# Kernel tuning notes

Hardware: AMD Instinct MI355X
Metric: run time of the kernel (lower is better)

The kernel has to match this reference:

```python
import jax, jax.numpy as jnp
import numpy as np

GAMMA, ZETA = -0.1, 1.1
N_BITS = 4
QMAX = (1 << N_BITS) - 1  # 15
OUT, IN, D, K = 4096, 4096, 8, 4096
L = (OUT * IN) // D  # 2097152 blocks, no padding needed


def setup_inputs() -> dict:
    key = jax.random.key(0)
    k = jax.random.split(key, 7)
    x = jax.random.normal(k[0], (4, 2048, IN), jnp.float32)
    codebook = jax.random.normal(k[1], (K, D), jnp.float32)
    indices = jax.random.randint(k[2], (L,), 0, K, jnp.int32)
    base_int = jax.random.randint(k[3], (OUT, IN), 0, QMAX, jnp.int32)
    scale = jax.random.uniform(k[4], (OUT, 1), jnp.float32)
    zero = jax.random.uniform(k[5], (OUT, 1), jnp.float32)
    bias = jax.random.normal(k[6], (OUT,), jnp.float32)
    return {"x": x, "codebook": codebook, "indices": indices,
            "base_int": base_int, "scale": scale, "zero": zero, "bias": bias}


def reference(x, codebook, indices, base_int, scale, zero, bias):
    # Gather codebook blocks and rebuild alpha with the weight's shape [OUT, IN]
    alpha = codebook[indices].reshape(OUT, IN)
    # Rectified sigmoid (soft quant mode)
    r = jnp.clip(jax.nn.sigmoid(alpha) * (ZETA - GAMMA) + GAMMA, 0.0, 1.0)
    # Affine int-quant reconstruction
    q_int = jnp.clip(base_int.astype(scale.dtype) + r + zero, 0.0, float(QMAX))
    Wq = scale * (q_int - zero)  # [OUT, IN]
    # F.linear: x @ Wq^T + bias
    return jnp.einsum('bsi,oi->bso', x, Wq) + bias
```

## Files before the change

kernel.cpp:

```cpp
#include <hip/hip_runtime.h>

#define M_DIM 8192
#define N_DIM 4096
#define K_DIM 4096
#define L_BLK 2097152
#define K2 8192

typedef __attribute__((ext_vector_type(8))) short short8;
typedef __attribute__((ext_vector_type(8))) unsigned short ushort8;
typedef __attribute__((ext_vector_type(4))) float f32x4;

__device__ __forceinline__ unsigned short f2bf(float f) {
  unsigned int u = __float_as_uint(f);
  unsigned int r = (u + 0x7fffu + ((u >> 16) & 1u)) >> 16;
  return (unsigned short)r;
}

__device__ __forceinline__ void gld16(const void* g, void* l) {
  __builtin_amdgcn_global_load_lds(
      (const __attribute__((address_space(1))) void*)g,
      (__attribute__((address_space(3))) void*)l, 16, 0, 0);
}

__global__ void dequant_kernel(const float* __restrict__ cb,
                               const int* __restrict__ idx,
                               const int* __restrict__ base,
                               const float* __restrict__ scale,
                               const float* __restrict__ zero,
                               unsigned short* __restrict__ W) {
  const int b = blockIdx.x * 256 + threadIdx.x;
  const int o = b >> 9;
  const float s = scale[o];
  const float z = zero[o];
  const int ci = idx[b];
  const float4* crow = (const float4*)(cb + (size_t)ci * 8);
  float4 c0 = crow[0], c1 = crow[1];
  const int4* brow = (const int4*)(base + (size_t)b * 8);
  int4 b0 = brow[0], b1 = brow[1];
  float a[8]  = {c0.x, c0.y, c0.z, c0.w, c1.x, c1.y, c1.z, c1.w};
  int   bi[8] = {b0.x, b0.y, b0.z, b0.w, b1.x, b1.y, b1.z, b1.w};
  union { unsigned short h[8]; ushort8 v; } u;
#pragma unroll
  for (int d = 0; d < 8; ++d) {
    float sg = 1.0f / (1.0f + __expf(-a[d]));
    float r = fminf(fmaxf(sg * 1.2f - 0.1f, 0.0f), 1.0f);
    float q = fminf(fmaxf((float)bi[d] + r + z, 0.0f), 15.0f);
    u.h[d] = f2bf(s * (q - z));
  }
  *(ushort8*)(W + (size_t)b * 8) = u.v;
}

__global__ void xconv_kernel(const float* __restrict__ x,
                             unsigned short* __restrict__ xb) {
  const size_t i = (size_t)blockIdx.x * 256 + threadIdx.x;
  const float4* X = (const float4*)x;
  float4 a0 = X[i * 2], a1 = X[i * 2 + 1];
  float f[8] = {a0.x, a0.y, a0.z, a0.w, a1.x, a1.y, a1.z, a1.w};
  union { unsigned short h[8]; ushort8 v; } u;
#pragma unroll
  for (int d = 0; d < 8; ++d) u.h[d] = f2bf(f[d]);
  *(ushort8*)(xb + i * 8) = u.v;
}


#define VMW(N) asm volatile("s_waitcnt vmcnt(" #N ")" ::: "memory")
#define BAR __builtin_amdgcn_s_barrier()

#define RDB(BF, BUFO) \
  _Pragma("unroll") for (int n = 0; n < 4; ++n) \
  _Pragma("unroll") for (int kk = 0; kk < 2; ++kk) \
    BF[n][kk] = *(const short8*)(lds + (BUFO) + 32768 + \
        (wn * 64 + n * 16 + r16) * 128 + (acol0 ^ (kk << 6)));

#define RDA(AF, BUFO, P) \
  _Pragma("unroll") for (int mi = 0; mi < 2; ++mi) \
  _Pragma("unroll") for (int kk = 0; kk < 2; ++kk) \
    AF[mi][kk] = *(const short8*)(lds + (BUFO) + \
        (wm * 128 + (2 * (P) + mi) * 16 + r16) * 128 + (acol0 ^ (kk << 6)));

#define FMQ(P, AF, BF) do { \
  __builtin_amdgcn_s_setprio(1); \
  _Pragma("unroll") for (int kk = 0; kk < 2; ++kk) \
  _Pragma("unroll") for (int mi = 0; mi < 2; ++mi) \
  _Pragma("unroll") for (int n = 0; n < 4; ++n) \
    acc[2 * (P) + mi][n] = __builtin_amdgcn_mfma_f32_16x16x32_bf16( \
        AF[mi][kk], BF[n][kk], acc[2 * (P) + mi][n], 0, 0, 0); \
  __builtin_amdgcn_s_setprio(0); \
} while (0)

#define ITER(CUR, NXT, T) do { \
   RDA(afA, CUR, 0); RDB(bf, CUR); \
  stA(NXT, 1, (T) + 1); stA(NXT, 3, (T) + 1); \
  BAR; FMQ(0, afA, bf); BAR; \
   RDA(afB, CUR, 1); \
  stB(CUR, 0, (T) + 2); stB(CUR, 1, (T) + 2); \
  BAR; FMQ(1, afB, bf); BAR; \
   RDA(afA, CUR, 2); \
  stB(CUR, 2, (T) + 2); stB(CUR, 3, (T) + 2); \
  BAR; FMQ(2, afA, bf); BAR; \
   RDA(afB, CUR, 3); \
  stA(CUR, 0, (T) + 2); stA(CUR, 2, (T) + 2); \
  VMW(6); BAR; FMQ(3, afB, bf); BAR; \
} while (0)

__global__ __launch_bounds__(512, 2)
void gemm_bt(const unsigned short* __restrict__ A,
             const unsigned short* __restrict__ B,
             const float* __restrict__ bias,
             float* __restrict__ C) {
  __shared__ char lds[131072];
  const int tid = threadIdx.x;
  const int lane = tid & 63;
  const int w = tid >> 6;
  const int wm = w >> 2;
  const int wn = w & 3;
  const int r16 = lane & 15;
  const int g = lane >> 4;
  const int acol0 = (g << 4) ^ ((r16 & 7) << 4);

  const int s = (int)blockIdx.x;
  const int wg = (s & 7) * 64 + (s >> 3);
  const int bm = wg & 31;
  const int bn = wg >> 5;

  const char* Abase = (const char*)A + (size_t)bm * 256 * K2;
  const char* Bbase = (const char*)B + (size_t)bn * 256 * K2;

  const int strow = tid >> 3;
  const int scol = ((tid & 7) * 16) ^ ((strow & 7) << 4);
  const int sdst = w * 1024;

  auto stA = [&](int bo, int c, int kt) {
    gld16(Abase + (size_t)(c * 64 + strow) * K2 + kt * 128 + scol,
          lds + bo + c * 8192 + sdst);
  };
  auto stB = [&](int bo, int c, int kt) {
    gld16(Bbase + (size_t)(c * 64 + strow) * K2 + kt * 128 + scol,
          lds + bo + 32768 + c * 8192 + sdst);
  };

  f32x4 acc[8][4] = {};
  short8 bf[4][2];
  short8 afA[2][2], afB[2][2];

  stB(0, 0, 0); stB(0, 1, 0); stB(0, 2, 0); stB(0, 3, 0);
  stA(0, 0, 0); stA(0, 1, 0); stA(0, 2, 0); stA(0, 3, 0);
  stB(65536, 0, 1); stB(65536, 1, 1); stB(65536, 2, 1); stB(65536, 3, 1);
  stA(65536, 0, 1); stA(65536, 2, 1);
  VMW(6); BAR;

  for (int tp = 0; tp < 31; ++tp) {
    ITER(0, 65536, 2 * tp);
    ITER(65536, 0, 2 * tp + 1);
  }
  RDA(afA, 0, 0); RDB(bf, 0);
  stA(65536, 1, 63); stA(65536, 3, 63);
  BAR; FMQ(0, afA, bf); BAR;
  RDA(afB, 0, 1);
  BAR; FMQ(1, afB, bf); BAR;
  RDA(afA, 0, 2);
  BAR; FMQ(2, afA, bf); BAR;
  RDA(afB, 0, 3);
  VMW(0); BAR; FMQ(3, afB, bf); BAR;
  RDA(afA, 65536, 0); RDB(bf, 65536);
  FMQ(0, afA, bf);
  RDA(afB, 65536, 1);
  FMQ(1, afB, bf);
  RDA(afA, 65536, 2);
  FMQ(2, afA, bf);
  RDA(afB, 65536, 3);
  FMQ(3, afB, bf);

  const int cb0 = bn * 256 + wn * 64 + r16;
  float bv[4];
#pragma unroll
  for (int n = 0; n < 4; ++n) bv[n] = bias[cb0 + n * 16];
#pragma unroll
  for (int m = 0; m < 8; ++m) {
#pragma unroll
    for (int j = 0; j < 4; ++j) {
      int row = bm * 256 + wm * 128 + m * 16 + g * 4 + j;
      float* Crow = C + (size_t)row * N_DIM + cb0;
#pragma unroll
      for (int n = 0; n < 4; ++n) Crow[n * 16] = acc[m][n][j] + bv[n];
    }
  }
}

extern "C" void kernel_launch(void* const* d_in, const int* in_sizes, int n_in,
                              void* d_out, int out_size, void* d_ws, size_t ws_size,
                              hipStream_t stream) {
  const float* x     = (const float*)d_in[0];
  const float* cb    = (const float*)d_in[1];
  const int*   idx   = (const int*)d_in[2];
  const int*   base  = (const int*)d_in[3];
  const float* scale = (const float*)d_in[4];
  const float* zero  = (const float*)d_in[5];
  const float* bias  = (const float*)d_in[6];
  float* out = (float*)d_out;

  unsigned short* Wq = (unsigned short*)d_ws;
  unsigned short* Xb = (unsigned short*)((char*)d_ws + (size_t)N_DIM * K_DIM * 2);

  dequant_kernel<<<L_BLK / 256, 256, 0, stream>>>(cb, idx, base, scale, zero, Wq);
  xconv_kernel<<<(M_DIM * K_DIM / 8) / 256, 256, 0, stream>>>(x, Xb);
  gemm_bt<<<(M_DIM / 256) * (N_DIM / 256), 512, 0, stream>>>(Xb, Wq, bias, out);
}
```

Baseline: 310.6 us.

## Merge prep kernels and switch GEMM to 4 waves with 128x128 warp tiles

Fuses the weight dequant and x bf16 conversion into one launch, which removes a kernel boundary. The GEMM drops from 8 waves to 4 per 256x256 tile. Each wave now computes a 128x128 sub-tile with 8x8 accumulators, and each thread issues two async global-to-LDS loads per stage. This raises per-wave register reuse of A/B fragments and cuts LDS read traffic per MFMA, at the cost of heavy VGPR pressure (256 accumulator floats) and fewer waves for hiding latency.

```diff
diff --git a/kernel.cpp b/kernel.cpp
--- a/kernel.cpp
+++ b/kernel.cpp
@@ -22,88 +22,89 @@
       (__attribute__((address_space(3))) void*)l, 16, 0, 0);
 }
 
-__global__ void dequant_kernel(const float* __restrict__ cb,
-                               const int* __restrict__ idx,
-                               const int* __restrict__ base,
-                               const float* __restrict__ scale,
-                               const float* __restrict__ zero,
-                               unsigned short* __restrict__ W) {
-  const int b = blockIdx.x * 256 + threadIdx.x;
-  const int o = b >> 9;
-  const float s = scale[o];
-  const float z = zero[o];
-  const int ci = idx[b];
-  const float4* crow = (const float4*)(cb + (size_t)ci * 8);
-  float4 c0 = crow[0], c1 = crow[1];
-  const int4* brow = (const int4*)(base + (size_t)b * 8);
-  int4 b0 = brow[0], b1 = brow[1];
-  float a[8]  = {c0.x, c0.y, c0.z, c0.w, c1.x, c1.y, c1.z, c1.w};
-  int   bi[8] = {b0.x, b0.y, b0.z, b0.w, b1.x, b1.y, b1.z, b1.w};
-  union { unsigned short h[8]; ushort8 v; } u;
-#pragma unroll
-  for (int d = 0; d < 8; ++d) {
-    float sg = 1.0f / (1.0f + __expf(-a[d]));
-    float r = fminf(fmaxf(sg * 1.2f - 0.1f, 0.0f), 1.0f);
-    float q = fminf(fmaxf((float)bi[d] + r + z, 0.0f), 15.0f);
-    u.h[d] = f2bf(s * (q - z));
+__global__ void prep_kernel(const float* __restrict__ cb,
+                            const int* __restrict__ idx,
+                            const int* __restrict__ base,
+                            const float* __restrict__ scale,
+                            const float* __restrict__ zero,
+                            const float* __restrict__ x,
+                            unsigned short* __restrict__ W,
+                            unsigned short* __restrict__ xb) {
+  if (blockIdx.x < L_BLK / 256) {
+    const int b = blockIdx.x * 256 + threadIdx.x;
+    const int o = b >> 9;
+    const float s = scale[o];
+    const float z = zero[o];
+    const int ci = idx[b];
+    const float4* crow = (const float4*)(cb + (size_t)ci * 8);
+    float4 c0 = crow[0], c1 = crow[1];
+    const int4* brow = (const int4*)(base + (size_t)b * 8);
+    int4 b0 = brow[0], b1 = brow[1];
+    float a[8]  = {c0.x, c0.y, c0.z, c0.w, c1.x, c1.y, c1.z, c1.w};
+    int   bi[8] = {b0.x, b0.y, b0.z, b0.w, b1.x, b1.y, b1.z, b1.w};
+    union { unsigned short h[8]; ushort8 v; } u;
+#pragma unroll
+    for (int d = 0; d < 8; ++d) {
+      float sg = 1.0f / (1.0f + __expf(-a[d]));
+      float r = fminf(fmaxf(sg * 1.2f - 0.1f, 0.0f), 1.0f);
+      float q = fminf(fmaxf((float)bi[d] + r + z, 0.0f), 15.0f);
+      u.h[d] = f2bf(s * (q - z));
+    }
+    *(ushort8*)(W + (size_t)b * 8) = u.v;
+  } else {
+    const size_t i = (size_t)(blockIdx.x - L_BLK / 256) * 256 + threadIdx.x;
+    const float4* X = (const float4*)x;
+    float4 a0 = X[i * 2], a1 = X[i * 2 + 1];
+    float f[8] = {a0.x, a0.y, a0.z, a0.w, a1.x, a1.y, a1.z, a1.w};
+    union { unsigned short h[8]; ushort8 v; } u;
+#pragma unroll
+    for (int d = 0; d < 8; ++d) u.h[d] = f2bf(f[d]);
+    *(ushort8*)(xb + i * 8) = u.v;
   }
-  *(ushort8*)(W + (size_t)b * 8) = u.v;
-}
-
-__global__ void xconv_kernel(const float* __restrict__ x,
-                             unsigned short* __restrict__ xb) {
-  const size_t i = (size_t)blockIdx.x * 256 + threadIdx.x;
-  const float4* X = (const float4*)x;
-  float4 a0 = X[i * 2], a1 = X[i * 2 + 1];
-  float f[8] = {a0.x, a0.y, a0.z, a0.w, a1.x, a1.y, a1.z, a1.w};
-  union { unsigned short h[8]; ushort8 v; } u;
-#pragma unroll
-  for (int d = 0; d < 8; ++d) u.h[d] = f2bf(f[d]);
-  *(ushort8*)(xb + i * 8) = u.v;
 }
 
 
 #define VMW(N) asm volatile("s_waitcnt vmcnt(" #N ")" ::: "memory")
 #define BAR __builtin_amdgcn_s_barrier()
 
-#define RDB(BF, BUFO) \
-  _Pragma("unroll") for (int n = 0; n < 4; ++n) \
+#define RDB_ALL(BUFO) \
+  _Pragma("unroll") for (int n = 0; n < 8; ++n) \
   _Pragma("unroll") for (int kk = 0; kk < 2; ++kk) \
-    BF[n][kk] = *(const short8*)(lds + (BUFO) + 32768 + \
-        (wn * 64 + n * 16 + r16) * 128 + (acol0 ^ (kk << 6)));
-
-#define RDA(AF, BUFO, P) \
+    bf[n][kk] = *(const short8*)(lds + (BUFO) + 32768 + \
+        (wn * 128 + n * 16 + r16) * 128 + (acol0 ^ (kk << 6)));
+
+#define RDA(BUFO, P) \
   _Pragma("unroll") for (int mi = 0; mi < 2; ++mi) \
   _Pragma("unroll") for (int kk = 0; kk < 2; ++kk) \
-    AF[mi][kk] = *(const short8*)(lds + (BUFO) + \
+    af[mi][kk] = *(const short8*)(lds + (BUFO) + \
         (wm * 128 + (2 * (P) + mi) * 16 + r16) * 128 + (acol0 ^ (kk << 6)));
 
-#define FMQ(P, AF, BF) do { \
+#define FMQ(P) do { \
   __builtin_amdgcn_s_setprio(1); \
   _Pragma("unroll") for (int kk = 0; kk < 2; ++kk) \
   _Pragma("unroll") for (int mi = 0; mi < 2; ++mi) \
-  _Pragma("unroll") for (int n = 0; n < 4; ++n) \
+  _Pragma("unroll") for (int n = 0; n < 8; ++n) \
     acc[2 * (P) + mi][n] = __builtin_amdgcn_mfma_f32_16x16x32_bf16( \
-        AF[mi][kk], BF[n][kk], acc[2 * (P) + mi][n], 0, 0, 0); \
+        af[mi][kk], bf[n][kk], acc[2 * (P) + mi][n], 0, 0, 0); \
   __builtin_amdgcn_s_setprio(0); \
 } while (0)
 
 #define ITER(CUR, NXT, T) do { \
-   RDA(afA, CUR, 0); RDB(bf, CUR); \
+   RDA(CUR, 0); RDB_ALL(CUR); \
   stA(NXT, 1, (T) + 1); stA(NXT, 3, (T) + 1); \
-  BAR; FMQ(0, afA, bf); BAR; \
-   RDA(afB, CUR, 1); \
+  BAR; FMQ(0); BAR; \
+   RDA(CUR, 1); \
   stB(CUR, 0, (T) + 2); stB(CUR, 1, (T) + 2); \
-  BAR; FMQ(1, afB, bf); BAR; \
-   RDA(afA, CUR, 2); \
+  BAR; FMQ(1); BAR; \
+   RDA(CUR, 2); \
   stB(CUR, 2, (T) + 2); stB(CUR, 3, (T) + 2); \
-  BAR; FMQ(2, afA, bf); BAR; \
-   RDA(afB, CUR, 3); \
+  BAR; FMQ(2); BAR; \
+   RDA(CUR, 3); \
   stA(CUR, 0, (T) + 2); stA(CUR, 2, (T) + 2); \
-  VMW(6); BAR; FMQ(3, afB, bf); BAR; \
+  VMW(12); BAR; FMQ(3); BAR; \
 } while (0)
 
-__global__ __launch_bounds__(512, 2)
+__global__ __launch_bounds__(256, 1)
 void gemm_bt(const unsigned short* __restrict__ A,
              const unsigned short* __restrict__ B,
              const float* __restrict__ bias,
@@ -112,8 +113,8 @@
   const int tid = threadIdx.x;
   const int lane = tid & 63;
   const int w = tid >> 6;
-  const int wm = w >> 2;
-  const int wn = w & 3;
+  const int wm = w >> 1;
+  const int wn = w & 1;
   const int r16 = lane & 15;
   const int g = lane >> 4;
   const int acol0 = (g << 4) ^ ((r16 & 7) << 4);
@@ -126,55 +127,58 @@
   const char* Abase = (const char*)A + (size_t)bm * 256 * K2;
   const char* Bbase = (const char*)B + (size_t)bn * 256 * K2;
 
-  const int strow = tid >> 3;
-  const int scol = ((tid & 7) * 16) ^ ((strow & 7) << 4);
-  const int sdst = w * 1024;
+  const int strow = (w << 3) + (lane >> 3);
+  const int scol = ((lane & 7) << 4) ^ ((lane >> 3) << 4);
 
   auto stA = [&](int bo, int c, int kt) {
-    gld16(Abase + (size_t)(c * 64 + strow) * K2 + kt * 128 + scol,
-          lds + bo + c * 8192 + sdst);
+    const char* src = Abase + (size_t)(c * 64 + strow) * K2 + kt * 128 + scol;
+    char* dst = lds + bo + c * 8192 + w * 1024;
+    gld16(src, dst);
+    gld16(src + (size_t)32 * K2, dst + 4096);
   };
   auto stB = [&](int bo, int c, int kt) {
-    gld16(Bbase + (size_t)(c * 64 + strow) * K2 + kt * 128 + scol,
-          lds + bo + 32768 + c * 8192 + sdst);
+    const char* src = Bbase + (size_t)(c * 64 + strow) * K2 + kt * 128 + scol;
+    char* dst = lds + bo + 32768 + c * 8192 + w * 1024;
+    gld16(src, dst);
+    gld16(src + (size_t)32 * K2, dst + 4096);
   };
 
-  f32x4 acc[8][4] = {};
-  short8 bf[4][2];
-  short8 afA[2][2], afB[2][2];
+  f32x4 acc[8][8] = {};
+  short8 bf[8][2];
+  short8 af[2][2];
 
   stB(0, 0, 0); stB(0, 1, 0); stB(0, 2, 0); stB(0, 3, 0);
   stA(0, 0, 0); stA(0, 1, 0); stA(0, 2, 0); stA(0, 3, 0);
   stB(65536, 0, 1); stB(65536, 1, 1); stB(65536, 2, 1); stB(65536, 3, 1);
   stA(65536, 0, 1); stA(65536, 2, 1);
-  VMW(6); BAR;
+  VMW(12); BAR;
 
   for (int tp = 0; tp < 31; ++tp) {
     ITER(0, 65536, 2 * tp);
     ITER(65536, 0, 2 * tp + 1);
   }
-  RDA(afA, 0, 0); RDB(bf, 0);
+  RDA(0, 0); RDB_ALL(0);
   stA(65536, 1, 63); stA(65536, 3, 63);
-  BAR; FMQ(0, afA, bf); BAR;
-  RDA(afB, 0, 1);
-  BAR; FMQ(1, afB, bf); BAR;
-  RDA(afA, 0, 2);
-  BAR; FMQ(2, afA, bf); BAR;
-  RDA(afB, 0, 3);
-  VMW(0); BAR; FMQ(3, afB, bf); BAR;
-  RDA(afA, 65536, 0); RDB(bf, 65536);
-  FMQ(0, afA, bf);
-  RDA(afB, 65536, 1);
-  FMQ(1, afB, bf);
-  RDA(afA, 65536, 2);
-  FMQ(2, afA, bf);
-  RDA(afB, 65536, 3);
-  FMQ(3, afB, bf);
-
-  const int cb0 = bn * 256 + wn * 64 + r16;
-  float bv[4];
-#pragma unroll
-  for (int n = 0; n < 4; ++n) bv[n] = bias[cb0 + n * 16];
+  BAR; FMQ(0); BAR;
+  RDA(0, 1);
+  BAR; FMQ(1); BAR;
+  RDA(0, 2);
+  BAR; FMQ(2); BAR;
+  RDA(0, 3);
+  VMW(0); BAR; FMQ(3); BAR;
+  RDA(65536, 0); RDB_ALL(65536);
+  FMQ(0);
+  RDA(65536, 1);
+  FMQ(1);
+  RDA(65536, 2);
+  FMQ(2);
+  RDA(65536, 3);
+  FMQ(3);
+
+  const int cb0 = bn * 256 + wn * 128 + r16;
+  float bv[8];
+#pragma unroll
+  for (int n = 0; n < 8; ++n) bv[n] = bias[cb0 + n * 16];
 #pragma unroll
   for (int m = 0; m < 8; ++m) {
 #pragma unroll
@@ -182,7 +186,7 @@
       int row = bm * 256 + wm * 128 + m * 16 + g * 4 + j;
       float* Crow = C + (size_t)row * N_DIM + cb0;
 #pragma unroll
-      for (int n = 0; n < 4; ++n) Crow[n * 16] = acc[m][n][j] + bv[n];
+      for (int n = 0; n < 8; ++n) Crow[n * 16] = acc[m][n][j] + bv[n];
     }
   }
 }
@@ -202,7 +206,7 @@
   unsigned short* Wq = (unsigned short*)d_ws;
   unsigned short* Xb = (unsigned short*)((char*)d_ws + (size_t)N_DIM * K_DIM * 2);
 
-  dequant_kernel<<<L_BLK / 256, 256, 0, stream>>>(cb, idx, base, scale, zero, Wq);
-  xconv_kernel<<<(M_DIM * K_DIM / 8) / 256, 256, 0, stream>>>(x, Xb);
-  gemm_bt<<<(M_DIM / 256) * (N_DIM / 256), 512, 0, stream>>>(Xb, Wq, bias, out);
-}
+  const int prep_blocks = L_BLK / 256 + (M_DIM * K_DIM / 8) / 256;
+  prep_kernel<<<prep_blocks, 256, 0, stream>>>(cb, idx, base, scale, zero, x, Wq, Xb);
+  gemm_bt<<<(M_DIM / 256) * (N_DIM / 256), 256, 0, stream>>>(Xb, Wq, bias, out);
+}
```

Measured after the change: 442.3 us. 42.4% more time.

## Switch GEMM to 32x32x16 MFMA tiles and merge prep kernels into one launch

Applied to the files above, without the earlier changes.

The GEMM inner loop moves from 16x16x32 bf16 MFMA to 32x32x16 bf16 MFMA. Each wave now holds a 4x2 grid of 32x32 accumulators, with the LDS fragment reads and the epilogue row mapping changed to match. The four compute phases per K-tile become two, which halves the barrier count and issues fewer, larger MFMAs. The weight-dequant and x-to-bf16 conversion kernels are fused into one launch split by block index, saving one kernel launch. The risks are different LDS bank-conflict patterns from the new read layout, and a less interleaved mix of global loads and compute with fewer phases.

```diff
diff --git a/kernel.cpp b/kernel.cpp
--- a/kernel.cpp
+++ b/kernel.cpp
@@ -8,7 +8,7 @@
 
 typedef __attribute__((ext_vector_type(8))) short short8;
 typedef __attribute__((ext_vector_type(8))) unsigned short ushort8;
-typedef __attribute__((ext_vector_type(4))) float f32x4;
+typedef __attribute__((ext_vector_type(16))) float f32x16;
 
 __device__ __forceinline__ unsigned short f2bf(float f) {
   unsigned int u = __float_as_uint(f);
@@ -22,85 +22,84 @@
       (__attribute__((address_space(3))) void*)l, 16, 0, 0);
 }
 
-__global__ void dequant_kernel(const float* __restrict__ cb,
-                               const int* __restrict__ idx,
-                               const int* __restrict__ base,
-                               const float* __restrict__ scale,
-                               const float* __restrict__ zero,
-                               unsigned short* __restrict__ W) {
-  const int b = blockIdx.x * 256 + threadIdx.x;
-  const int o = b >> 9;
-  const float s = scale[o];
-  const float z = zero[o];
-  const int ci = idx[b];
-  const float4* crow = (const float4*)(cb + (size_t)ci * 8);
-  float4 c0 = crow[0], c1 = crow[1];
-  const int4* brow = (const int4*)(base + (size_t)b * 8);
-  int4 b0 = brow[0], b1 = brow[1];
-  float a[8]  = {c0.x, c0.y, c0.z, c0.w, c1.x, c1.y, c1.z, c1.w};
-  int   bi[8] = {b0.x, b0.y, b0.z, b0.w, b1.x, b1.y, b1.z, b1.w};
-  union { unsigned short h[8]; ushort8 v; } u;
+__global__ void prep_kernel(const float* __restrict__ cb,
+                            const int* __restrict__ idx,
+                            const int* __restrict__ base,
+                            const float* __restrict__ scale,
+                            const float* __restrict__ zero,
+                            const float* __restrict__ x,
+                            unsigned short* __restrict__ W,
+                            unsigned short* __restrict__ xb) {
+  if (blockIdx.x < L_BLK / 256) {
+    const int b = blockIdx.x * 256 + threadIdx.x;
+    const int o = b >> 9;
+    const float s = scale[o];
+    const float z = zero[o];
+    const int ci = idx[b];
+    const float4* crow = (const float4*)(cb + (size_t)ci * 8);
+    float4 c0 = crow[0], c1 = crow[1];
+    const int4* brow = (const int4*)(base + (size_t)b * 8);
+    int4 b0 = brow[0], b1 = brow[1];
+    float a[8]  = {c0.x, c0.y, c0.z, c0.w, c1.x, c1.y, c1.z, c1.w};
+    int   bi[8] = {b0.x, b0.y, b0.z, b0.w, b1.x, b1.y, b1.z, b1.w};
+    union { unsigned short h[8]; ushort8 v; } u;
 #pragma unroll
-  for (int d = 0; d < 8; ++d) {
-    float sg = 1.0f / (1.0f + __expf(-a[d]));
-    float r = fminf(fmaxf(sg * 1.2f - 0.1f, 0.0f), 1.0f);
-    float q = fminf(fmaxf((float)bi[d] + r + z, 0.0f), 15.0f);
-    u.h[d] = f2bf(s * (q - z));
+    for (int d = 0; d < 8; ++d) {
+      float sg = 1.0f / (1.0f + __expf(-a[d]));
+      float r = fminf(fmaxf(sg * 1.2f - 0.1f, 0.0f), 1.0f);
+      float q = fminf(fmaxf((float)bi[d] + r + z, 0.0f), 15.0f);
+      u.h[d] = f2bf(s * (q - z));
+    }
+    *(ushort8*)(W + (size_t)b * 8) = u.v;
+  } else {
+    const size_t i = (size_t)(blockIdx.x - L_BLK / 256) * 256 + threadIdx.x;
+    const float4* X = (const float4*)x;
+    float4 a0 = X[i * 2], a1 = X[i * 2 + 1];
+    float f[8] = {a0.x, a0.y, a0.z, a0.w, a1.x, a1.y, a1.z, a1.w};
+    union { unsigned short h[8]; ushort8 v; } u;
+#pragma unroll
+    for (int d = 0; d < 8; ++d) u.h[d] = f2bf(f[d]);
+    *(ushort8*)(xb + i * 8) = u.v;
   }
-  *(ushort8*)(W + (size_t)b * 8) = u.v;
-}
-
-__global__ void xconv_kernel(const float* __restrict__ x,
-                             unsigned short* __restrict__ xb) {
-  const size_t i = (size_t)blockIdx.x * 256 + threadIdx.x;
-  const float4* X = (const float4*)x;
-  float4 a0 = X[i * 2], a1 = X[i * 2 + 1];
-  float f[8] = {a0.x, a0.y, a0.z, a0.w, a1.x, a1.y, a1.z, a1.w};
-  union { unsigned short h[8]; ushort8 v; } u;
-#pragma unroll
-  for (int d = 0; d < 8; ++d) u.h[d] = f2bf(f[d]);
-  *(ushort8*)(xb + i * 8) = u.v;
 }
 
 
 #define VMW(N) asm volatile("s_waitcnt vmcnt(" #N ")" ::: "memory")
 #define BAR __builtin_amdgcn_s_barrier()
 
-#define RDB(BF, BUFO) \
-  _Pragma("unroll") for (int n = 0; n < 4; ++n) \
-  _Pragma("unroll") for (int kk = 0; kk < 2; ++kk) \
-    BF[n][kk] = *(const short8*)(lds + (BUFO) + 32768 + \
-        (wn * 64 + n * 16 + r16) * 128 + (acol0 ^ (kk << 6)));
+#define RDB(BUFO) \
+  _Pragma("unroll") for (int nf = 0; nf < 2; ++nf) \
+  _Pragma("unroll") for (int ks = 0; ks < 4; ++ks) \
+    bf[nf][ks] = *(const short8*)(lds + (BUFO) + 32768 + \
+        (wn * 64 + nf * 32 + l31) * 128 + ((ks * 32 + h16) ^ swz));
 
-#define RDA(AF, BUFO, P) \
+#define RDA2(BUFO, MF) \
   _Pragma("unroll") for (int mi = 0; mi < 2; ++mi) \
-  _Pragma("unroll") for (int kk = 0; kk < 2; ++kk) \
-    AF[mi][kk] = *(const short8*)(lds + (BUFO) + \
-        (wm * 128 + (2 * (P) + mi) * 16 + r16) * 128 + (acol0 ^ (kk << 6)));
+  _Pragma("unroll") for (int ks = 0; ks < 4; ++ks) \
+    af[mi][ks] = *(const short8*)(lds + (BUFO) + \
+        (wm * 128 + ((MF) + mi) * 32 + l31) * 128 + ((ks * 32 + h16) ^ swz));
 
-#define FMQ(P, AF, BF) do { \
+#define FM2(MF) do { \
   __builtin_amdgcn_s_setprio(1); \
-  _Pragma("unroll") for (int kk = 0; kk < 2; ++kk) \
+  _Pragma("unroll") for (int ks = 0; ks < 4; ++ks) \
   _Pragma("unroll") for (int mi = 0; mi < 2; ++mi) \
-  _Pragma("unroll") for (int n = 0; n < 4; ++n) \
-    acc[2 * (P) + mi][n] = __builtin_amdgcn_mfma_f32_16x16x32_bf16( \
-        AF[mi][kk], BF[n][kk], acc[2 * (P) + mi][n], 0, 0, 0); \
+  _Pragma("unroll") for (int nf = 0; nf < 2; ++nf) \
+    acc[(MF) + mi][nf] = __builtin_amdgcn_mfma_f32_32x32x16_bf16( \
+        af[mi][ks], bf[nf][ks], acc[(MF) + mi][nf], 0, 0, 0); \
   __builtin_amdgcn_s_setprio(0); \
 } while (0)
 
 #define ITER(CUR, NXT, T) do { \
-   RDA(afA, CUR, 0); RDB(bf, CUR); \
+   \
+  RDB(CUR); RDA2(CUR, 0); \
   stA(NXT, 1, (T) + 1); stA(NXT, 3, (T) + 1); \
-  BAR; FMQ(0, afA, bf); BAR; \
-   RDA(afB, CUR, 1); \
+  BAR; FM2(0); BAR; \
+   \
+  RDA2(CUR, 2); \
   stB(CUR, 0, (T) + 2); stB(CUR, 1, (T) + 2); \
-  BAR; FMQ(1, afB, bf); BAR; \
-   RDA(afA, CUR, 2); \
   stB(CUR, 2, (T) + 2); stB(CUR, 3, (T) + 2); \
-  BAR; FMQ(2, afA, bf); BAR; \
-   RDA(afB, CUR, 3); \
   stA(CUR, 0, (T) + 2); stA(CUR, 2, (T) + 2); \
-  VMW(6); BAR; FMQ(3, afB, bf); BAR; \
+  VMW(6); BAR; FM2(2); BAR; \
 } while (0)
 
 __global__ __launch_bounds__(512, 2)
@@ -114,9 +113,9 @@
   const int w = tid >> 6;
   const int wm = w >> 2;
   const int wn = w & 3;
-  const int r16 = lane & 15;
-  const int g = lane >> 4;
-  const int acol0 = (g << 4) ^ ((r16 & 7) << 4);
+  const int l31 = lane & 31;
+  const int h16 = (lane >> 5) * 16;
+  const int swz = (l31 & 7) << 4;
 
   const int s = (int)blockIdx.x;
   const int wg = (s & 7) * 64 + (s >> 3);
@@ -139,9 +138,9 @@
           lds + bo + 32768 + c * 8192 + sdst);
   };
 
-  f32x4 acc[8][4] = {};
-  short8 bf[4][2];
-  short8 afA[2][2], afB[2][2];
+  f32x16 acc[4][2] = {};
+  short8 bf[2][4];
+  short8 af[2][4];
 
   stB(0, 0, 0); stB(0, 1, 0); stB(0, 2, 0); stB(0, 3, 0);
   stA(0, 0, 0); stA(0, 1, 0); stA(0, 2, 0); stA(0, 3, 0);
@@ -153,36 +152,28 @@
     ITER(0, 65536, 2 * tp);
     ITER(65536, 0, 2 * tp + 1);
   }
-  RDA(afA, 0, 0); RDB(bf, 0);
+  RDB(0); RDA2(0, 0);
   stA(65536, 1, 63); stA(65536, 3, 63);
-  BAR; FMQ(0, afA, bf); BAR;
-  RDA(afB, 0, 1);
-  BAR; FMQ(1, afB, bf); BAR;
-  RDA(afA, 0, 2);
-  BAR; FMQ(2, afA, bf); BAR;
-  RDA(afB, 0, 3);
-  VMW(0); BAR; FMQ(3, afB, bf); BAR;
-  RDA(afA, 65536, 0); RDB(bf, 65536);
-  FMQ(0, afA, bf);
-  RDA(afB, 65536, 1);
-  FMQ(1, afB, bf);
-  RDA(afA, 65536, 2);
-  FMQ(2, afA, bf);
-  RDA(afB, 65536, 3);
-  FMQ(3, afB, bf);
+  BAR; FM2(0); BAR;
+  RDA2(0, 2);
+  VMW(0); BAR; FM2(2); BAR;
+  RDB(65536); RDA2(65536, 0);
+  FM2(0);
+  RDA2(65536, 2);
+  FM2(2);
 
-  const int cb0 = bn * 256 + wn * 64 + r16;
-  float bv[4];
+  const int cb0 = bn * 256 + wn * 64 + l31;
+  const int hr = (lane >> 5) * 2;
+  float bv0 = bias[cb0];
+  float bv1 = bias[cb0 + 32];
 #pragma unroll
-  for (int n = 0; n < 4; ++n) bv[n] = bias[cb0 + n * 16];
+  for (int mf = 0; mf < 4; ++mf) {
 #pragma unroll
-  for (int m = 0; m < 8; ++m) {
-#pragma unroll
-    for (int j = 0; j < 4; ++j) {
-      int row = bm * 256 + wm * 128 + m * 16 + g * 4 + j;
+    for (int r = 0; r < 16; ++r) {
+      int row = bm * 256 + wm * 128 + mf * 32 + (r & 3) + 8 * (r >> 2) + 2 * hr;
       float* Crow = C + (size_t)row * N_DIM + cb0;
-#pragma unroll
-      for (int n = 0; n < 4; ++n) Crow[n * 16] = acc[m][n][j] + bv[n];
+      Crow[0]  = acc[mf][0][r] + bv0;
+      Crow[32] = acc[mf][1][r] + bv1;
     }
   }
 }
@@ -202,7 +193,7 @@
   unsigned short* Wq = (unsigned short*)d_ws;
   unsigned short* Xb = (unsigned short*)((char*)d_ws + (size_t)N_DIM * K_DIM * 2);
 
-  dequant_kernel<<<L_BLK / 256, 256, 0, stream>>>(cb, idx, base, scale, zero, Wq);
-  xconv_kernel<<<(M_DIM * K_DIM / 8) / 256, 256, 0, stream>>>(x, Xb);
+  const int prep_blocks = L_BLK / 256 + (M_DIM * K_DIM / 8) / 256;
+  prep_kernel<<<prep_blocks, 256, 0, stream>>>(cb, idx, base, scale, zero, x, Wq, Xb);
   gemm_bt<<<(M_DIM / 256) * (N_DIM / 256), 512, 0, stream>>>(Xb, Wq, bias, out);
 }
```

Measured after the change: 343.7 us. +10.6%, slower.

## Merge prep kernels and restructure GEMM into 2x2 quadrant MFMA schedule

Applied to the files above, without the earlier changes.

The dequant and x-conversion kernels are merged into one launch that picks its job from the block index, which removes one kernel launch and the gap between the two. The GEMM inner loop now works in 2x2 quadrants: four A fragments with two B fragments per phase instead of two A with four B. All B loads for the next tile are issued in the first phase, and explicit lgkmcnt waits are added. This changes register use and the point at which global-to-LDS prefetches are issued. There is some risk in the buffer-reuse timing and the reduced B prefetch depth.

```diff
diff --git a/kernel.cpp b/kernel.cpp
--- a/kernel.cpp
+++ b/kernel.cpp
@@ -22,85 +22,91 @@
       (__attribute__((address_space(3))) void*)l, 16, 0, 0);
 }
 
-__global__ void dequant_kernel(const float* __restrict__ cb,
-                               const int* __restrict__ idx,
-                               const int* __restrict__ base,
-                               const float* __restrict__ scale,
-                               const float* __restrict__ zero,
-                               unsigned short* __restrict__ W) {
-  const int b = blockIdx.x * 256 + threadIdx.x;
-  const int o = b >> 9;
-  const float s = scale[o];
-  const float z = zero[o];
-  const int ci = idx[b];
-  const float4* crow = (const float4*)(cb + (size_t)ci * 8);
-  float4 c0 = crow[0], c1 = crow[1];
-  const int4* brow = (const int4*)(base + (size_t)b * 8);
-  int4 b0 = brow[0], b1 = brow[1];
-  float a[8]  = {c0.x, c0.y, c0.z, c0.w, c1.x, c1.y, c1.z, c1.w};
-  int   bi[8] = {b0.x, b0.y, b0.z, b0.w, b1.x, b1.y, b1.z, b1.w};
-  union { unsigned short h[8]; ushort8 v; } u;
-#pragma unroll
-  for (int d = 0; d < 8; ++d) {
-    float sg = 1.0f / (1.0f + __expf(-a[d]));
-    float r = fminf(fmaxf(sg * 1.2f - 0.1f, 0.0f), 1.0f);
-    float q = fminf(fmaxf((float)bi[d] + r + z, 0.0f), 15.0f);
-    u.h[d] = f2bf(s * (q - z));
+__global__ void prep_kernel(const float* __restrict__ cb,
+                            const int* __restrict__ idx,
+                            const int* __restrict__ base,
+                            const float* __restrict__ scale,
+                            const float* __restrict__ zero,
+                            const float* __restrict__ x,
+                            unsigned short* __restrict__ W,
+                            unsigned short* __restrict__ xb) {
+  if (blockIdx.x < L_BLK / 256) {
+    const int b = blockIdx.x * 256 + threadIdx.x;
+    const int o = b >> 9;
+    const float s = scale[o];
+    const float z = zero[o];
+    const int ci = idx[b];
+    const float4* crow = (const float4*)(cb + (size_t)ci * 8);
+    float4 c0 = crow[0], c1 = crow[1];
+    const int4* brow = (const int4*)(base + (size_t)b * 8);
+    int4 b0 = brow[0], b1 = brow[1];
+    float a[8]  = {c0.x, c0.y, c0.z, c0.w, c1.x, c1.y, c1.z, c1.w};
+    int   bi[8] = {b0.x, b0.y, b0.z, b0.w, b1.x, b1.y, b1.z, b1.w};
+    union { unsigned short h[8]; ushort8 v; } u;
+#pragma unroll
+    for (int d = 0; d < 8; ++d) {
+      float sg = 1.0f / (1.0f + __expf(-a[d]));
+      float r = fminf(fmaxf(sg * 1.2f - 0.1f, 0.0f), 1.0f);
+      float q = fminf(fmaxf((float)bi[d] + r + z, 0.0f), 15.0f);
+      u.h[d] = f2bf(s * (q - z));
+    }
+    *(ushort8*)(W + (size_t)b * 8) = u.v;
+  } else {
+    const size_t i = (size_t)(blockIdx.x - L_BLK / 256) * 256 + threadIdx.x;
+    const float4* X = (const float4*)x;
+    float4 a0 = X[i * 2], a1 = X[i * 2 + 1];
+    float f[8] = {a0.x, a0.y, a0.z, a0.w, a1.x, a1.y, a1.z, a1.w};
+    union { unsigned short h[8]; ushort8 v; } u;
+#pragma unroll
+    for (int d = 0; d < 8; ++d) u.h[d] = f2bf(f[d]);
+    *(ushort8*)(xb + i * 8) = u.v;
   }
-  *(ushort8*)(W + (size_t)b * 8) = u.v;
-}
-
-__global__ void xconv_kernel(const float* __restrict__ x,
-                             unsigned short* __restrict__ xb) {
-  const size_t i = (size_t)blockIdx.x * 256 + threadIdx.x;
-  const float4* X = (const float4*)x;
-  float4 a0 = X[i * 2], a1 = X[i * 2 + 1];
-  float f[8] = {a0.x, a0.y, a0.z, a0.w, a1.x, a1.y, a1.z, a1.w};
-  union { unsigned short h[8]; ushort8 v; } u;
-#pragma unroll
-  for (int d = 0; d < 8; ++d) u.h[d] = f2bf(f[d]);
-  *(ushort8*)(xb + i * 8) = u.v;
 }
 
 
 #define VMW(N) asm volatile("s_waitcnt vmcnt(" #N ")" ::: "memory")
+#define LGKM8 asm volatile("s_waitcnt lgkmcnt(8)" ::: "memory")
 #define BAR __builtin_amdgcn_s_barrier()
 
-#define RDB(BF, BUFO) \
-  _Pragma("unroll") for (int n = 0; n < 4; ++n) \
+#define RDA4(BUFO, MH) \
+  _Pragma("unroll") for (int mi = 0; mi < 4; ++mi) \
   _Pragma("unroll") for (int kk = 0; kk < 2; ++kk) \
-    BF[n][kk] = *(const short8*)(lds + (BUFO) + 32768 + \
-        (wn * 64 + n * 16 + r16) * 128 + (acol0 ^ (kk << 6)));
-
-#define RDA(AF, BUFO, P) \
-  _Pragma("unroll") for (int mi = 0; mi < 2; ++mi) \
+    af[mi][kk] = *(const short8*)(lds + (BUFO) + \
+        (wm * 128 + ((MH) * 4 + mi) * 16 + r16) * 128 + (acol0 ^ (kk << 6)));
+
+#define RDB2(BUFO, NH) \
+  _Pragma("unroll") for (int ni = 0; ni < 2; ++ni) \
   _Pragma("unroll") for (int kk = 0; kk < 2; ++kk) \
-    AF[mi][kk] = *(const short8*)(lds + (BUFO) + \
-        (wm * 128 + (2 * (P) + mi) * 16 + r16) * 128 + (acol0 ^ (kk << 6)));
-
-#define FMQ(P, AF, BF) do { \
+    bf[ni][kk] = *(const short8*)(lds + (BUFO) + 32768 + \
+        (wn * 64 + ((NH) * 2 + ni) * 16 + r16) * 128 + (acol0 ^ (kk << 6)));
+
+#define FMQ2(MH, NH) do { \
   __builtin_amdgcn_s_setprio(1); \
   _Pragma("unroll") for (int kk = 0; kk < 2; ++kk) \
-  _Pragma("unroll") for (int mi = 0; mi < 2; ++mi) \
-  _Pragma("unroll") for (int n = 0; n < 4; ++n) \
-    acc[2 * (P) + mi][n] = __builtin_amdgcn_mfma_f32_16x16x32_bf16( \
-        AF[mi][kk], BF[n][kk], acc[2 * (P) + mi][n], 0, 0, 0); \
+  _Pragma("unroll") for (int mi = 0; mi < 4; ++mi) \
+  _Pragma("unroll") for (int ni = 0; ni < 2; ++ni) \
+    acc[(MH) * 4 + mi][(NH) * 2 + ni] = __builtin_amdgcn_mfma_f32_16x16x32_bf16( \
+        af[mi][kk], bf[ni][kk], acc[(MH) * 4 + mi][(NH) * 2 + ni], 0, 0, 0); \
   __builtin_amdgcn_s_setprio(0); \
 } while (0)
 
 #define ITER(CUR, NXT, T) do { \
-   RDA(afA, CUR, 0); RDB(bf, CUR); \
+   \
+  RDA4(CUR, 0); RDB2(CUR, 0); \
+  stB(NXT, 0, (T) + 1); stB(NXT, 1, (T) + 1); \
+  stB(NXT, 2, (T) + 1); stB(NXT, 3, (T) + 1); \
   stA(NXT, 1, (T) + 1); stA(NXT, 3, (T) + 1); \
-  BAR; FMQ(0, afA, bf); BAR; \
-   RDA(afB, CUR, 1); \
-  stB(CUR, 0, (T) + 2); stB(CUR, 1, (T) + 2); \
-  BAR; FMQ(1, afB, bf); BAR; \
-   RDA(afA, CUR, 2); \
-  stB(CUR, 2, (T) + 2); stB(CUR, 3, (T) + 2); \
-  BAR; FMQ(2, afA, bf); BAR; \
-   RDA(afB, CUR, 3); \
+  LGKM8; BAR; FMQ2(0, 0); BAR; \
+   \
+  RDB2(CUR, 1); \
+  BAR; FMQ2(0, 1); BAR; \
+   \
+  RDA4(CUR, 1); RDB2(CUR, 0); \
   stA(CUR, 0, (T) + 2); stA(CUR, 2, (T) + 2); \
-  VMW(6); BAR; FMQ(3, afB, bf); BAR; \
+  LGKM8; BAR; FMQ2(1, 0); BAR; \
+   \
+  RDB2(CUR, 1); \
+  VMW(2); BAR; FMQ2(1, 1); BAR; \
 } while (0)
 
 __global__ __launch_bounds__(512, 2)
@@ -140,36 +146,37 @@
   };
 
   f32x4 acc[8][4] = {};
-  short8 bf[4][2];
-  short8 afA[2][2], afB[2][2];
+  short8 af[4][2];
+  short8 bf[2][2];
 
   stB(0, 0, 0); stB(0, 1, 0); stB(0, 2, 0); stB(0, 3, 0);
   stA(0, 0, 0); stA(0, 1, 0); stA(0, 2, 0); stA(0, 3, 0);
-  stB(65536, 0, 1); stB(65536, 1, 1); stB(65536, 2, 1); stB(65536, 3, 1);
   stA(65536, 0, 1); stA(65536, 2, 1);
-  VMW(6); BAR;
+  VMW(2); BAR;
 
   for (int tp = 0; tp < 31; ++tp) {
     ITER(0, 65536, 2 * tp);
     ITER(65536, 0, 2 * tp + 1);
   }
-  RDA(afA, 0, 0); RDB(bf, 0);
+  RDA4(0, 0); RDB2(0, 0);
+  stB(65536, 0, 63); stB(65536, 1, 63);
+  stB(65536, 2, 63); stB(65536, 3, 63);
   stA(65536, 1, 63); stA(65536, 3, 63);
-  BAR; FMQ(0, afA, bf); BAR;
-  RDA(afB, 0, 1);
-  BAR; FMQ(1, afB, bf); BAR;
-  RDA(afA, 0, 2);
-  BAR; FMQ(2, afA, bf); BAR;
-  RDA(afB, 0, 3);
-  VMW(0); BAR; FMQ(3, afB, bf); BAR;
-  RDA(afA, 65536, 0); RDB(bf, 65536);
-  FMQ(0, afA, bf);
-  RDA(afB, 65536, 1);
-  FMQ(1, afB, bf);
-  RDA(afA, 65536, 2);
-  FMQ(2, afA, bf);
-  RDA(afB, 65536, 3);
-  FMQ(3, afB, bf);
+  LGKM8; BAR; FMQ2(0, 0); BAR;
+  RDB2(0, 1);
+  BAR; FMQ2(0, 1); BAR;
+  RDA4(0, 1); RDB2(0, 0);
+  LGKM8; BAR; FMQ2(1, 0); BAR;
+  RDB2(0, 1);
+  VMW(0); BAR; FMQ2(1, 1); BAR;
+  RDA4(65536, 0); RDB2(65536, 0);
+  FMQ2(0, 0);
+  RDB2(65536, 1);
+  FMQ2(0, 1);
+  RDA4(65536, 1); RDB2(65536, 0);
+  FMQ2(1, 0);
+  RDB2(65536, 1);
+  FMQ2(1, 1);
 
   const int cb0 = bn * 256 + wn * 64 + r16;
   float bv[4];
@@ -202,7 +209,7 @@
   unsigned short* Wq = (unsigned short*)d_ws;
   unsigned short* Xb = (unsigned short*)((char*)d_ws + (size_t)N_DIM * K_DIM * 2);
 
-  dequant_kernel<<<L_BLK / 256, 256, 0, stream>>>(cb, idx, base, scale, zero, Wq);
-  xconv_kernel<<<(M_DIM * K_DIM / 8) / 256, 256, 0, stream>>>(x, Xb);
+  const int prep_blocks = L_BLK / 256 + (M_DIM * K_DIM / 8) / 256;
+  prep_kernel<<<prep_blocks, 256, 0, stream>>>(cb, idx, base, scale, zero, x, Wq, Xb);
   gemm_bt<<<(M_DIM / 256) * (N_DIM / 256), 512, 0, stream>>>(Xb, Wq, bias, out);
 }
```

After: 321.1 us. 3.4% more time.
